# Optimization experiments

Measured on AMD Instinct MI355X. Metric: run time of the kernel, lower is better.

The kernel has to match this reference:

```python
import jax, jax.numpy as jnp
import numpy as np

# MACE symmetric contraction, element-dependent, correlation=3, scalar (0e) output.
B, C, L, E = 8192, 128, 16, 10     # atoms, feature channels, sum(2l+1) for lmax=3, elements
K1, K2, K3 = 1, 4, 23              # U-matrix path counts per correlation order


def _sparse_U(key, shape, density):
    # Clebsch-Gordan-like tensors are highly sparse/structured; emulate with masked randn.
    kv, km = jax.random.split(key)
    mask = jax.random.bernoulli(km, density, shape)
    return jnp.where(mask, jax.random.normal(kv, shape), 0.0).astype(jnp.float32)


def setup_inputs() -> dict:
    key = jax.random.key(0)
    ks = jax.random.split(key, 8)
    U1 = _sparse_U(ks[0], (L, K1), 0.5)          # (i, k1)
    U2 = _sparse_U(ks[1], (L, L, K2), 0.12)      # (p, i, k2)
    U3 = _sparse_U(ks[2], (L, L, L, K3), 0.12)   # (p, q, i, k3)
    W1 = (jax.random.normal(ks[3], (E, K1, C)) / K1).astype(jnp.float32)
    W2 = (jax.random.normal(ks[4], (E, K2, C)) / K2).astype(jnp.float32)
    W3 = (jax.random.normal(ks[5], (E, K3, C)) / K3).astype(jnp.float32)
    x = jax.random.normal(ks[6], (B, C, L), dtype=jnp.float32)
    y = jax.random.uniform(ks[7], (B, E), dtype=jnp.float32)  # element attribute vector
    return {"x": x, "y": y, "U1": U1, "U2": U2, "U3": U3, "W1": W1, "W2": W2, "W3": W3}


def reference(x, y, U1, U2, U3, W1, W2, W3):
    # correlation = 3 main contraction: '...ik,ekc,bci,be->bc...'
    out = jnp.einsum('pqik,ekc,bci,be->bcpq', U3, W3, x, y)      # (B, C, L, L)
    # corr = 2: weighting '...k,ekc,be->bc...' then contract 'bc...i,bci->bc...'
    c2 = jnp.einsum('pik,ekc,be->bcpi', U2, W2, y) + out          # (B, C, L, L)
    out = jnp.einsum('bcpi,bci->bcp', c2, x)                      # (B, C, L)
    # corr = 1
    c1 = jnp.einsum('ik,ekc,be->bci', U1, W1, y) + out            # (B, C, L)
    out = jnp.einsum('bci,bci->bc', c1, x)                        # (B, C)
    return out  # already flattened: (B, C)
```

## Files before the change

### kernel.cpp

```cpp
#include <hip/hip_runtime.h>
#include <hip/hip_bf16.h>
#include <stdint.h>

#define B_ATOMS 8192
#define C_CH    128
#define L_DIM   16
#define E_EL    10
#define NK3     23
#define NK2     4
#define NTRI    136
#define KPAD    160
#define NCOL    384
#define KSB     336
#define TSE     136

#define XX_OFF  0
#define XB_OFF  43008
#define XT_OFF  47104
#define WT_OFF  51728
#define WS_OFF  62336
#define SMEM_BYTES 64384

typedef __attribute__((ext_vector_type(8))) short short8;
typedef __attribute__((ext_vector_type(4))) float f32x4;

struct TriLut { unsigned char p[NTRI]; unsigned char q[NTRI]; };
static constexpr TriLut make_lut() {
  TriLut t{};
  int idx = 0;
  for (int p = 0; p < 16; ++p)
    for (int q = p; q < 16; ++q) { t.p[idx] = (unsigned char)p; t.q[idx] = (unsigned char)q; ++idx; }
  return t;
}
__constant__ TriLut LUT = make_lut();

__device__ __forceinline__ unsigned short f2bf(float f) {
  union { float f; unsigned u; } v; v.f = f;
  unsigned r = v.u + 0x7fffu + ((v.u >> 16) & 1u);
  return (unsigned short)(r >> 16);
}
__device__ __forceinline__ unsigned pack2(float a, float b) {
  __hip_bfloat162 h = __float22bfloat162_rn(float2{a, b});
  union { __hip_bfloat162 h; unsigned u; } v; v.h = h;
  return v.u;
}
__device__ __forceinline__ float bf2f(unsigned short h) {
  union { unsigned u; float f; } v; v.u = ((unsigned)h) << 16;
  return v.f;
}
__device__ __forceinline__ float2 bfup(unsigned u) {
  float2 r;
  r.x = __uint_as_float(u << 16);
  r.y = __uint_as_float(u & 0xffff0000u);
  return r;
}
template <int CTRL>
__device__ __forceinline__ float dpp_add(float s) {
  int v = __builtin_amdgcn_update_dpp(0, __float_as_int(s), CTRL, 0xf, 0xf, true);
  return s + __int_as_float(v);
}
__device__ __forceinline__ float row16_sum(float s) {
  s = dpp_add<0x111>(s);
  s = dpp_add<0x112>(s);
  s = dpp_add<0x114>(s);
  s = dpp_add<0x118>(s);
  return s;
}

__global__ void build_bt(const float* __restrict__ U1, const float* __restrict__ U2,
                         const float* __restrict__ U3, unsigned short* __restrict__ bt) {
  int gid = blockIdx.x * 256 + threadIdx.x;
  if (gid >= NCOL * KPAD) return;
  int n  = gid / KPAD;
  int kk = gid - n * KPAD;
  float val = 0.f;
  if (kk < NTRI && n < 372) {
    int p = LUT.p[kk], q = LUT.q[kk];
    if (n < 368) {
      int i = n / NK3, k3 = n - i * NK3;
      val = U3[((p * 16 + q) * 16 + i) * NK3 + k3];
      if (p != q) val += U3[((q * 16 + p) * 16 + i) * NK3 + k3];
    } else {
      int k2 = n - 368;
      val = U2[(p * 16 + q) * NK2 + k2];
      if (p != q) val += U2[(q * 16 + p) * NK2 + k2];
    }
  } else if (n == 372 && kk >= 136 && kk < 152) {
    val = U1[kk - 136];
  }
  bt[gid] = f2bf(val);
}

template <bool FIRST>
__device__ __forceinline__ void do_pass(const char* __restrict__ smem, float* __restrict__ ws,
                                        const unsigned short* __restrict__ bt,
                                        int nbase, int w, int l16, int quad) {
  short8 bfrag[3][5];
#pragma unroll
  for (int nt = 0; nt < 3; ++nt) {
    const unsigned short* src = bt + (size_t)(nbase + nt * 16 + l16) * KPAD + quad * 8;
#pragma unroll
    for (int ks = 0; ks < 5; ++ks)
      bfrag[nt][ks] = *(const short8*)(src + ks * 32);
  }
  f32x4 acc[8][3];
#pragma unroll
  for (int mt = 0; mt < 8; ++mt)
#pragma unroll
    for (int nt = 0; nt < 3; ++nt) acc[mt][nt] = (f32x4){0.f, 0.f, 0.f, 0.f};
#pragma unroll
  for (int ks = 0; ks < 5; ++ks) {
    short8 af[8];
#pragma unroll
    for (int mt = 0; mt < 8; ++mt)
      af[mt] = *(const short8*)(smem + XX_OFF + (mt * 16 + l16) * KSB + ks * 64 + quad * 16);
#pragma unroll
    for (int nt = 0; nt < 3; ++nt)
#pragma unroll
      for (int mt = 0; mt < 8; ++mt)
        acc[mt][nt] = __builtin_amdgcn_mfma_f32_16x16x32_bf16(af[mt], bfrag[nt][ks], acc[mt][nt], 0, 0, 0);
  }
  int ktab[3], irow[3];
#pragma unroll
  for (int nt = 0; nt < 3; ++nt) {
    const int n = nbase + nt * 16 + l16;
    const int i = n / NK3;
    irow[nt] = i;
    ktab[nt] = (n < 368) ? (n - i * NK3) : (n - 345);
  }
  const unsigned short* xt = (const unsigned short*)(smem + XT_OFF);
  const unsigned short* wt = (const unsigned short*)(smem + WT_OFF);
#pragma unroll
  for (int mt = 0; mt < 8; ++mt) {
    const int c4 = mt * 16 + quad * 4;
    float s0 = 0.f, s1 = 0.f, s2 = 0.f, s3 = 0.f;
#pragma unroll
    for (int nt = 0; nt < 3; ++nt) {
      uint2 wv = *(const uint2*)(wt + ktab[nt] * TSE + c4);
      uint2 xv = *(const uint2*)(xt + irow[nt] * TSE + c4);
      float2 w01 = bfup(wv.x), w23 = bfup(wv.y);
      float2 x01 = bfup(xv.x), x23 = bfup(xv.y);
      s0 += acc[mt][nt][0] * (w01.x * x01.x);
      s1 += acc[mt][nt][1] * (w01.y * x01.y);
      s2 += acc[mt][nt][2] * (w23.x * x23.x);
      s3 += acc[mt][nt][3] * (w23.y * x23.y);
    }
    s0 = row16_sum(s0);
    s1 = row16_sum(s1);
    s2 = row16_sum(s2);
    s3 = row16_sum(s3);
    if (l16 == 15) {
      float* dst = ws + w * C_CH + c4;
      if (FIRST) {
        *(float4*)dst = (float4){s0, s1, s2, s3};
      } else {
        float4 old = *(const float4*)dst;
        *(float4*)dst = (float4){old.x + s0, old.y + s1, old.z + s2, old.w + s3};
      }
    }
  }
}

__global__ __launch_bounds__(256, 2) void mace_main(
    const float* __restrict__ x, const float* __restrict__ y,
    const float* __restrict__ W1, const float* __restrict__ W2,
    const float* __restrict__ W3,
    const unsigned short* __restrict__ bt, float* __restrict__ out) {
  __shared__ __align__(16) char smem[SMEM_BYTES];
  const int t  = threadIdx.x;
  const int b  = blockIdx.x;
  const int lane = t & 63, w = t >> 6;
  const int quad = lane >> 4, l16 = lane & 15;

  {
    const float4* x4 = (const float4*)(x + (size_t)b * C_CH * L_DIM);
    unsigned short* xtb = (unsigned short*)(smem + XT_OFF);
#pragma unroll
    for (int r = 0; r < 2; ++r) {
      const int o = t + r * 256;
      float4 f = x4[o];
      const int c = o >> 2, i0 = (o & 3) * 4;
      unsigned* xb = (unsigned*)((unsigned short*)(smem + XB_OFF) + c * 16 + i0);
      xb[0] = pack2(f.x, f.y);
      xb[1] = pack2(f.z, f.w);
      xtb[(i0 + 0) * TSE + c] = f2bf(f.x);
      xtb[(i0 + 1) * TSE + c] = f2bf(f.y);
      xtb[(i0 + 2) * TSE + c] = f2bf(f.z);
      xtb[(i0 + 3) * TSE + c] = f2bf(f.w);
    }
    if (t < C_CH) xtb[16 * TSE + t] = 0x3f80;
  }
  {
    float yv[E_EL];
#pragma unroll
    for (int e = 0; e < E_EL; ++e) yv[e] = y[(size_t)b * E_EL + e];
    unsigned short* wtb = (unsigned short*)(smem + WT_OFF);
    for (int u = t; u < 39 * 32; u += 256) {
      const int k = u >> 5, cg = (u & 31) * 4;
      float4 a = {0.f, 0.f, 0.f, 0.f};
      if (k < 23) {
#pragma unroll
        for (int e = 0; e < E_EL; ++e) {
          float4 wv = *(const float4*)(W3 + (e * NK3 + k) * C_CH + cg);
          a.x += yv[e] * wv.x; a.y += yv[e] * wv.y; a.z += yv[e] * wv.z; a.w += yv[e] * wv.w;
        }
      } else if (k < 27) {
#pragma unroll
        for (int e = 0; e < E_EL; ++e) {
          float4 wv = *(const float4*)(W2 + (e * NK2 + (k - 23)) * C_CH + cg);
          a.x += yv[e] * wv.x; a.y += yv[e] * wv.y; a.z += yv[e] * wv.z; a.w += yv[e] * wv.w;
        }
      } else if (k == 27) {
#pragma unroll
        for (int e = 0; e < E_EL; ++e) {
          float4 wv = *(const float4*)(W1 + e * C_CH + cg);
          a.x += yv[e] * wv.x; a.y += yv[e] * wv.y; a.z += yv[e] * wv.z; a.w += yv[e] * wv.w;
        }
      }
      uint2 pw;
      pw.x = pack2(a.x, a.y);
      pw.y = pack2(a.z, a.w);
      *(uint2*)(wtb + k * TSE + cg) = pw;
    }
  }
  __syncthreads();
  {
    const int c = t >> 1, half = t & 1;
    const unsigned short* xr = (const unsigned short*)(smem + XB_OFF) + c * 16;
    short8 x0 = *(const short8*)(xr);
    short8 x1 = *(const short8*)(xr + 8);
    float xf[16];
#pragma unroll
    for (int i = 0; i < 8; ++i) {
      xf[i]     = bf2f((unsigned short)x0[i]);
      xf[i + 8] = bf2f((unsigned short)x1[i]);
    }
    unsigned* dst = (unsigned*)(smem + XX_OFF + c * KSB);
    float prev = 0.f;
    int idx = 0;
#pragma unroll
    for (int p = 0; p < 16; ++p) {
#pragma unroll
      for (int q = p; q < 16; ++q) {
        const bool mine = (idx < 68) == (half == 0);
        if (mine) {
          const float val = xf[p] * xf[q];
          if (idx & 1) dst[idx >> 1] = pack2(prev, val);
          else prev = val;
        }
        ++idx;
      }
    }
    if (half) {
      const unsigned* xp = (const unsigned*)xr;
#pragma unroll
      for (int j = 0; j < 8; ++j) dst[68 + j] = xp[j];
#pragma unroll
      for (int j = 76; j < 80; ++j) dst[j] = 0u;
    }
  }
  __syncthreads();
  float* ws = (float*)(smem + WS_OFF);
  do_pass<true >(smem, ws, bt, w * 96,      w, l16, quad);
  do_pass<false>(smem, ws, bt, w * 96 + 48, w, l16, quad);
  __syncthreads();
  if (t < C_CH) {
    float s = ws[t] + ws[C_CH + t] + ws[2 * C_CH + t] + ws[3 * C_CH + t];
    out[(size_t)b * C_CH + t] = s;
  }
}

extern "C" void kernel_launch(void* const* d_in, const int* in_sizes, int n_in,
                              void* d_out, int out_size, void* d_ws, size_t ws_size,
                              hipStream_t stream) {
  const float* x  = (const float*)d_in[0];
  const float* y  = (const float*)d_in[1];
  const float* U1 = (const float*)d_in[2];
  const float* U2 = (const float*)d_in[3];
  const float* U3 = (const float*)d_in[4];
  const float* W1 = (const float*)d_in[5];
  const float* W2 = (const float*)d_in[6];
  const float* W3 = (const float*)d_in[7];
  float* out = (float*)d_out;
  unsigned short* bt = (unsigned short*)d_ws;
  if (ws_size < (size_t)NCOL * KPAD * sizeof(unsigned short)) return;

  build_bt<<<dim3((NCOL * KPAD + 255) / 256), dim3(256), 0, stream>>>(U1, U2, U3, bt);
  mace_main<<<dim3(B_ATOMS), dim3(256), 0, stream>>>(x, y, W1, W2, W3, bt, out);
}
```

Baseline: 304.4 us.

## Split channels across two blocks per atom to shrink LDS and raise occupancy

Each atom is now handled by two blocks of 64 channels each instead of one block of 128, which cuts shared memory per block roughly in half and lets the launch bounds ask for 4 blocks per CU. The x staging now reads x straight from global and builds the pairwise products in the same step, dropping the intermediate bf16 buffer and one barrier. Half the threads do x preprocessing while the other half build the element-weighted W table at the same time. B fragments are software-pipelined one k-step ahead instead of all being preloaded, which lowers register pressure. In exchange the bt fragments are loaded twice per atom and the W and y loads are duplicated across the two blocks.

```diff
diff --git a/kernel.cpp b/kernel.cpp
--- a/kernel.cpp
+++ b/kernel.cpp
@@ -4,6 +4,7 @@
 
 #define B_ATOMS 8192
 #define C_CH    128
+#define CHB     64
 #define L_DIM   16
 #define E_EL    10
 #define NK3     23
@@ -12,14 +13,13 @@
 #define KPAD    160
 #define NCOL    384
 #define KSB     336
-#define TSE     136
+#define TSE     72
 
 #define XX_OFF  0
-#define XB_OFF  43008
-#define XT_OFF  47104
-#define WT_OFF  51728
-#define WS_OFF  62336
-#define SMEM_BYTES 64384
+#define XT_OFF  21504
+#define WT_OFF  23952
+#define WS_OFF  28128
+#define SMEM_BYTES 29152
 
 typedef __attribute__((ext_vector_type(8))) short short8;
 typedef __attribute__((ext_vector_type(4))) float f32x4;
@@ -43,10 +43,6 @@
   __hip_bfloat162 h = __float22bfloat162_rn(float2{a, b});
   union { __hip_bfloat162 h; unsigned u; } v; v.h = h;
   return v.u;
-}
-__device__ __forceinline__ float bf2f(unsigned short h) {
-  union { unsigned u; float f; } v; v.u = ((unsigned)h) << 16;
-  return v.f;
 }
 __device__ __forceinline__ float2 bfup(unsigned u) {
   float2 r;
@@ -95,43 +91,52 @@
 __device__ __forceinline__ void do_pass(const char* __restrict__ smem, float* __restrict__ ws,
                                         const unsigned short* __restrict__ bt,
                                         int nbase, int w, int l16, int quad) {
-  short8 bfrag[3][5];
-#pragma unroll
-  for (int nt = 0; nt < 3; ++nt) {
-    const unsigned short* src = bt + (size_t)(nbase + nt * 16 + l16) * KPAD + quad * 8;
-#pragma unroll
-    for (int ks = 0; ks < 5; ++ks)
-      bfrag[nt][ks] = *(const short8*)(src + ks * 32);
-  }
-  f32x4 acc[8][3];
-#pragma unroll
-  for (int mt = 0; mt < 8; ++mt)
+  const unsigned short* bp[3];
+#pragma unroll
+  for (int nt = 0; nt < 3; ++nt)
+    bp[nt] = bt + (size_t)(nbase + nt * 16 + l16) * KPAD + quad * 8;
+
+  short8 bcur[3], bnxt[3];
+#pragma unroll
+  for (int nt = 0; nt < 3; ++nt) bcur[nt] = *(const short8*)(bp[nt]);
+
+  f32x4 acc[4][3];
+#pragma unroll
+  for (int mt = 0; mt < 4; ++mt)
 #pragma unroll
     for (int nt = 0; nt < 3; ++nt) acc[mt][nt] = (f32x4){0.f, 0.f, 0.f, 0.f};
+
 #pragma unroll
   for (int ks = 0; ks < 5; ++ks) {
-    short8 af[8];
-#pragma unroll
-    for (int mt = 0; mt < 8; ++mt)
+    if (ks < 4) {
+#pragma unroll
+      for (int nt = 0; nt < 3; ++nt) bnxt[nt] = *(const short8*)(bp[nt] + (ks + 1) * 32);
+    }
+    short8 af[4];
+#pragma unroll
+    for (int mt = 0; mt < 4; ++mt)
       af[mt] = *(const short8*)(smem + XX_OFF + (mt * 16 + l16) * KSB + ks * 64 + quad * 16);
 #pragma unroll
     for (int nt = 0; nt < 3; ++nt)
 #pragma unroll
-      for (int mt = 0; mt < 8; ++mt)
-        acc[mt][nt] = __builtin_amdgcn_mfma_f32_16x16x32_bf16(af[mt], bfrag[nt][ks], acc[mt][nt], 0, 0, 0);
-  }
+      for (int mt = 0; mt < 4; ++mt)
+        acc[mt][nt] = __builtin_amdgcn_mfma_f32_16x16x32_bf16(af[mt], bcur[nt], acc[mt][nt], 0, 0, 0);
+#pragma unroll
+    for (int nt = 0; nt < 3; ++nt) bcur[nt] = bnxt[nt];
+  }
+
   int ktab[3], irow[3];
 #pragma unroll
   for (int nt = 0; nt < 3; ++nt) {
     const int n = nbase + nt * 16 + l16;
     const int i = n / NK3;
     irow[nt] = i;
-    ktab[nt] = (n < 368) ? (n - i * NK3) : (n - 345);
+    ktab[nt] = (n < 368) ? (n - i * NK3) : min(n - 345, 28);
   }
   const unsigned short* xt = (const unsigned short*)(smem + XT_OFF);
   const unsigned short* wt = (const unsigned short*)(smem + WT_OFF);
 #pragma unroll
-  for (int mt = 0; mt < 8; ++mt) {
+  for (int mt = 0; mt < 4; ++mt) {
     const int c4 = mt * 16 + quad * 4;
     float s0 = 0.f, s1 = 0.f, s2 = 0.f, s3 = 0.f;
 #pragma unroll
@@ -150,7 +155,7 @@
     s2 = row16_sum(s2);
     s3 = row16_sum(s3);
     if (l16 == 15) {
-      float* dst = ws + w * C_CH + c4;
+      float* dst = ws + w * CHB + c4;
       if (FIRST) {
         *(float4*)dst = (float4){s0, s1, s2, s3};
       } else {
@@ -161,80 +166,27 @@
   }
 }
 
-__global__ __launch_bounds__(256, 2) void mace_main(
+__global__ __launch_bounds__(256, 4) void mace_main(
     const float* __restrict__ x, const float* __restrict__ y,
     const float* __restrict__ W1, const float* __restrict__ W2,
     const float* __restrict__ W3,
     const unsigned short* __restrict__ bt, float* __restrict__ out) {
   __shared__ __align__(16) char smem[SMEM_BYTES];
   const int t  = threadIdx.x;
-  const int b  = blockIdx.x;
+  const int b  = blockIdx.y;
+  const int ch0 = blockIdx.x * CHB;
   const int lane = t & 63, w = t >> 6;
   const int quad = lane >> 4, l16 = lane & 15;
 
-  {
-    const float4* x4 = (const float4*)(x + (size_t)b * C_CH * L_DIM);
+  if (t < 128) {
+    const int c = t >> 1, half = t & 1;
+    const float4* xs = (const float4*)(x + ((size_t)b * C_CH + ch0 + c) * L_DIM);
+    float4 f0 = xs[0], f1 = xs[1], f2 = xs[2], f3 = xs[3];
+    float xf[16] = {f0.x, f0.y, f0.z, f0.w, f1.x, f1.y, f1.z, f1.w,
+                    f2.x, f2.y, f2.z, f2.w, f3.x, f3.y, f3.z, f3.w};
     unsigned short* xtb = (unsigned short*)(smem + XT_OFF);
 #pragma unroll
-    for (int r = 0; r < 2; ++r) {
-      const int o = t + r * 256;
-      float4 f = x4[o];
-      const int c = o >> 2, i0 = (o & 3) * 4;
-      unsigned* xb = (unsigned*)((unsigned short*)(smem + XB_OFF) + c * 16 + i0);
-      xb[0] = pack2(f.x, f.y);
-      xb[1] = pack2(f.z, f.w);
-      xtb[(i0 + 0) * TSE + c] = f2bf(f.x);
-      xtb[(i0 + 1) * TSE + c] = f2bf(f.y);
-      xtb[(i0 + 2) * TSE + c] = f2bf(f.z);
-      xtb[(i0 + 3) * TSE + c] = f2bf(f.w);
-    }
-    if (t < C_CH) xtb[16 * TSE + t] = 0x3f80;
-  }
-  {
-    float yv[E_EL];
-#pragma unroll
-    for (int e = 0; e < E_EL; ++e) yv[e] = y[(size_t)b * E_EL + e];
-    unsigned short* wtb = (unsigned short*)(smem + WT_OFF);
-    for (int u = t; u < 39 * 32; u += 256) {
-      const int k = u >> 5, cg = (u & 31) * 4;
-      float4 a = {0.f, 0.f, 0.f, 0.f};
-      if (k < 23) {
-#pragma unroll
-        for (int e = 0; e < E_EL; ++e) {
-          float4 wv = *(const float4*)(W3 + (e * NK3 + k) * C_CH + cg);
-          a.x += yv[e] * wv.x; a.y += yv[e] * wv.y; a.z += yv[e] * wv.z; a.w += yv[e] * wv.w;
-        }
-      } else if (k < 27) {
-#pragma unroll
-        for (int e = 0; e < E_EL; ++e) {
-          float4 wv = *(const float4*)(W2 + (e * NK2 + (k - 23)) * C_CH + cg);
-          a.x += yv[e] * wv.x; a.y += yv[e] * wv.y; a.z += yv[e] * wv.z; a.w += yv[e] * wv.w;
-        }
-      } else if (k == 27) {
-#pragma unroll
-        for (int e = 0; e < E_EL; ++e) {
-          float4 wv = *(const float4*)(W1 + e * C_CH + cg);
-          a.x += yv[e] * wv.x; a.y += yv[e] * wv.y; a.z += yv[e] * wv.z; a.w += yv[e] * wv.w;
-        }
-      }
-      uint2 pw;
-      pw.x = pack2(a.x, a.y);
-      pw.y = pack2(a.z, a.w);
-      *(uint2*)(wtb + k * TSE + cg) = pw;
-    }
-  }
-  __syncthreads();
-  {
-    const int c = t >> 1, half = t & 1;
-    const unsigned short* xr = (const unsigned short*)(smem + XB_OFF) + c * 16;
-    short8 x0 = *(const short8*)(xr);
-    short8 x1 = *(const short8*)(xr + 8);
-    float xf[16];
-#pragma unroll
-    for (int i = 0; i < 8; ++i) {
-      xf[i]     = bf2f((unsigned short)x0[i]);
-      xf[i + 8] = bf2f((unsigned short)x1[i]);
-    }
+    for (int i = 0; i < 8; ++i) xtb[(half * 8 + i) * TSE + c] = f2bf(xf[half * 8 + i]);
     unsigned* dst = (unsigned*)(smem + XX_OFF + c * KSB);
     float prev = 0.f;
     int idx = 0;
@@ -252,11 +204,45 @@
       }
     }
     if (half) {
-      const unsigned* xp = (const unsigned*)xr;
-#pragma unroll
-      for (int j = 0; j < 8; ++j) dst[68 + j] = xp[j];
+#pragma unroll
+      for (int j = 0; j < 8; ++j) dst[68 + j] = pack2(xf[2 * j], xf[2 * j + 1]);
 #pragma unroll
       for (int j = 76; j < 80; ++j) dst[j] = 0u;
+    }
+  } else {
+    const int tt = t - 128;
+    unsigned short* xtb = (unsigned short*)(smem + XT_OFF);
+    if (tt < CHB) xtb[16 * TSE + tt] = 0x3f80;
+    float yv[E_EL];
+#pragma unroll
+    for (int e = 0; e < E_EL; ++e) yv[e] = y[(size_t)b * E_EL + e];
+    unsigned short* wtb = (unsigned short*)(smem + WT_OFF);
+    for (int u = tt; u < 29 * 16; u += 128) {
+      const int k = u >> 4, cg = (u & 15) * 4;
+      float4 a = {0.f, 0.f, 0.f, 0.f};
+      if (k < 23) {
+#pragma unroll
+        for (int e = 0; e < E_EL; ++e) {
+          float4 wv = *(const float4*)(W3 + (e * NK3 + k) * C_CH + ch0 + cg);
+          a.x += yv[e] * wv.x; a.y += yv[e] * wv.y; a.z += yv[e] * wv.z; a.w += yv[e] * wv.w;
+        }
+      } else if (k < 27) {
+#pragma unroll
+        for (int e = 0; e < E_EL; ++e) {
+          float4 wv = *(const float4*)(W2 + (e * NK2 + (k - 23)) * C_CH + ch0 + cg);
+          a.x += yv[e] * wv.x; a.y += yv[e] * wv.y; a.z += yv[e] * wv.z; a.w += yv[e] * wv.w;
+        }
+      } else if (k == 27) {
+#pragma unroll
+        for (int e = 0; e < E_EL; ++e) {
+          float4 wv = *(const float4*)(W1 + e * C_CH + ch0 + cg);
+          a.x += yv[e] * wv.x; a.y += yv[e] * wv.y; a.z += yv[e] * wv.z; a.w += yv[e] * wv.w;
+        }
+      }
+      uint2 pw;
+      pw.x = pack2(a.x, a.y);
+      pw.y = pack2(a.z, a.w);
+      *(uint2*)(wtb + k * TSE + cg) = pw;
     }
   }
   __syncthreads();
@@ -264,9 +250,9 @@
   do_pass<true >(smem, ws, bt, w * 96,      w, l16, quad);
   do_pass<false>(smem, ws, bt, w * 96 + 48, w, l16, quad);
   __syncthreads();
-  if (t < C_CH) {
-    float s = ws[t] + ws[C_CH + t] + ws[2 * C_CH + t] + ws[3 * C_CH + t];
-    out[(size_t)b * C_CH + t] = s;
+  if (t < CHB) {
+    float s = ws[t] + ws[CHB + t] + ws[2 * CHB + t] + ws[3 * CHB + t];
+    out[(size_t)b * C_CH + ch0 + t] = s;
   }
 }
 
@@ -286,5 +272,5 @@
   if (ws_size < (size_t)NCOL * KPAD * sizeof(unsigned short)) return;
 
   build_bt<<<dim3((NCOL * KPAD + 255) / 256), dim3(256), 0, stream>>>(U1, U2, U3, bt);
-  mace_main<<<dim3(B_ATOMS), dim3(256), 0, stream>>>(x, y, W1, W2, W3, bt, out);
-}
+  mace_main<<<dim3(2, B_ATOMS), dim3(256), 0, stream>>>(x, y, W1, W2, W3, bt, out);
+}
```

After: 296.6 us. -2.6%, faster.
